# Kernel tuning notes

Hardware: AMD Instinct MI355X
Metric: run time of the kernel (lower is better)

Reference implementation:

```python
import jax, jax.numpy as jnp
import numpy as np

K = 4          # torus_dim (circles)
M = 6          # n_modes
GRID = 12      # grid_size for Laplacian eigenvalues
T = 2.0        # uniformity temperature
SPREAD_W = 1.0
B = 8192       # batch size


def _karmonic_weights():
    # lambda_n = 2 - 2 cos(2 pi n / N), n = 1..M; w = (lam - lam1)/(lam_max - lam1)
    n = np.arange(1, M + 1)
    lam = 2.0 - 2.0 * np.cos(2.0 * np.pi * n / GRID)
    w = (lam - lam[0]) / (lam.max() - lam[0])
    return jnp.asarray(w, dtype=jnp.float32)


def setup_inputs() -> dict:
    key = jax.random.key(0)
    k1, k2 = jax.random.split(key)
    angles = jax.random.normal(k1, (B, K), dtype=jnp.float32)
    fourier_embed = jax.random.normal(k2, (B, 2 * K * M), dtype=jnp.float32)
    return {"angles": angles, "fourier_embed": fourier_embed}


def reference(angles, fourier_embed):
    Bn = fourier_embed.shape[0]
    w = _karmonic_weights()
    # group by mode: (B, M, 2K)
    x = fourier_embed.reshape(Bn, M, 2 * K)
    eye = jnp.eye(Bn, dtype=bool)
    log_Bm1 = jnp.log(jnp.float32(Bn - 1))

    total_unif = jnp.float32(0.0)
    mode_unifs = []
    for n in range(M):  # fixed small structural loop over modes
        xn = x[:, n, :]                                   # (B, 2K)
        sq = jnp.sum(xn * xn, axis=1)                     # (B,)
        d2 = sq[:, None] + sq[None, :] - 2.0 * (xn @ xn.T)
        d2 = jnp.maximum(d2, 0.0)                         # cdist(...)**2, clamped >= 0
        neg = jnp.where(eye, -jnp.inf, -T * d2)           # exclude diagonal like masked_select
        unif_n = jnp.mean(jax.nn.logsumexp(neg, axis=1)) - log_Bm1
        mode_unifs.append(unif_n)
        total_unif = total_unif + w[n] * unif_n

    # circular decorrelation (spread) across circle pairs, vectorized over pairs
    mu = jnp.arctan2(jnp.mean(jnp.sin(angles), axis=0),
                     jnp.mean(jnp.cos(angles), axis=0))   # (K,) circular means
    s = jnp.sin(angles - mu[None, :])                     # (B, K)
    cov = (s.T @ s) / jnp.float32(Bn)                     # (K, K) = mean(s_i * s_j)
    var = jnp.diagonal(cov)                               # mean(s_i^2)
    den = jnp.sqrt(var[:, None] * var[None, :] + 1e-8)
    corr2 = (cov / den) ** 2
    iu = np.triu_indices(K, 1)                            # upper-triangle pairs i<j
    spread = jnp.mean(corr2[iu])

    total = total_unif + jnp.float32(SPREAD_W) * spread
    return total_unif, spread, total, jnp.stack(mode_unifs)
```

## Files before the change

### kernel.cpp

```cpp
#include <hip/hip_runtime.h>
#include <math.h>

constexpr int BN = 8192;
constexpr int MN = 6;

constexpr float TL    = 2.8853900817779268f;
constexpr float SCL_Z = 2.4022448795936154f;

typedef __bf16 bf16_t;
typedef bf16_t bf16x8 __attribute__((ext_vector_type(8)));
typedef float f32x4 __attribute__((ext_vector_type(4)));

union PK { bf16_t h[8]; uint4 u; };

__device__ __forceinline__ bf16x8 frag_of(uint4 u) {
    return __builtin_bit_cast(bf16x8, u);
}

__device__ __host__ __forceinline__ int midx(int a, int b) {
    return 8 * a - (a * (a - 1)) / 2 + (b - a);
}


__global__ __launch_bounds__(256) void prep_ang(const float* __restrict__ x,
                                                const float* __restrict__ ang,
                                                uint4* __restrict__ C,
                                                float* __restrict__ angp) {
    const int blk = blockIdx.x;
    const int tid = threadIdx.x;
    if (blk < 192) {
        int idx = blk * 256 + tid;
        int n = idx >> 13;
        int j = idx & (BN - 1);
        const float* p = x + (size_t)j * 48 + n * 8;

        PK zh, zl, a3, b3;
        float sq = 0.f;
#pragma unroll
        for (int k = 0; k < 8; ++k) {
            float v = p[k];
            sq = fmaf(v, v, sq);
            float z = SCL_Z * v;
            bf16_t h = (bf16_t)z;
            zh.h[k] = h;
            zl.h[k] = (bf16_t)(z - (float)h);
        }
        float s = -TL * sq;
        bf16_t sh = (bf16_t)s;
        bf16_t sl = (bf16_t)(s - (float)sh);
        bf16_t one = (bf16_t)1.0f, zero = (bf16_t)0.0f;
        a3.h[0] = one; a3.h[1] = one; a3.h[2] = sh;  a3.h[3] = sl;
        b3.h[0] = sh;  b3.h[1] = sl;  b3.h[2] = one; b3.h[3] = one;
#pragma unroll
        for (int k = 4; k < 8; ++k) { a3.h[k] = zero; b3.h[k] = zero; }

        size_t base = ((size_t)(n * 512 + (j >> 4))) * 64 + (j & 15);
        C[base +  0] = zh.u;
        C[base + 16] = zl.u;
        C[base + 32] = a3.u;
        C[base + 48] = b3.u;
    } else {
        const int i = (blk - 192) * 256 + tid;
        float v[8];
#pragma unroll
        for (int k = 0; k < 4; ++k) __sincosf(ang[i * 4 + k], &v[k], &v[4 + k]);
        float acc[44];
        int c = 0;
#pragma unroll
        for (int a = 0; a < 8; ++a)
#pragma unroll
            for (int bq = a; bq < 8; ++bq) acc[c++] = v[a] * v[bq];
#pragma unroll
        for (int a = 0; a < 8; ++a) acc[36 + a] = v[a];

#pragma unroll
        for (int q = 0; q < 44; ++q) {
            float s = acc[q];
            s += __shfl_xor(s, 1);  s += __shfl_xor(s, 2);
            s += __shfl_xor(s, 4);  s += __shfl_xor(s, 8);
            s += __shfl_xor(s, 16); s += __shfl_xor(s, 32);
            acc[q] = s;
        }
        __shared__ float sm[4][44];
        const int w = tid >> 6, lane = tid & 63;
        if (lane == 0)
#pragma unroll
            for (int q = 0; q < 44; ++q) sm[w][q] = acc[q];
        __syncthreads();
        if (tid < 44)
            angp[(blk - 192) * 44 + tid] =
                sm[0][tid] + sm[1][tid] + sm[2][tid] + sm[3][tid];
    }
}

__global__ __launch_bounds__(512, 6) void pair_sweep(const uint4* __restrict__ C,
                                                     float* __restrict__ colsumP,
                                                     unsigned short* __restrict__ credP) {
    const int tid  = threadIdx.x;
    const int lane = tid & 63;
    const int w    = __builtin_amdgcn_readfirstlane(tid >> 6);
    const int b    = blockIdx.x;
    const int m    = b >> 7;
    const int sp   = (b >> 1) & 63;
    const int h    = b & 1;
    const int rho  = 2 * w + h;

    __shared__ float cred[8192];
    __shared__ float smem[2][8][64];
    for (int q = tid; q < 8192; q += 512) cred[q] = 0.f;
    __syncthreads();

    const int g  = lane >> 4;
    const int pa = (g == 3) ? 2 : (g & 1);
    const int pb = (g == 3) ? 3 : (g >> 1);
    const int cl = lane & 15;
    const f32x4 z4 = {0.f, 0.f, 0.f, 0.f};
    const uint4* mbase = C + (size_t)m * 512 * 64;
    const uint4* bcol  = mbase + pb * 16 + cl;

#pragma unroll 1
    for (int sidx = 0; sidx < 2; ++sidx) {
        const int s = sidx ? (127 - sp) : sp;

        bf16x8 af[4];
#pragma unroll
        for (int t = 0; t < 4; ++t)
            af[t] = frag_of(mbase[(size_t)(4 * s + t) * 64 + pa * 16 + cl]);

        float racc[16];
#pragma unroll
        for (int q = 0; q < 16; ++q) racc[q] = 0.f;

        const int start = 4 * s + 4;
        const int first = start + (int)(((unsigned)(rho - start)) & 15u);
        const int f0 = (first < 512) ? first : 0;

        uint4 b0 = bcol[(size_t)f0 * 64];
        uint4 b1 = bcol[(size_t)(f0 + 16) * 64];
        for (int jt = first; jt < 512; jt += 16) {
            uint4 p0 = bcol[(size_t)(jt + 32) * 64];
            bf16x8 bf = frag_of(b0);
            float rsum = 0.f;
#pragma unroll
            for (int t = 0; t < 4; ++t) {
                f32x4 d = __builtin_amdgcn_mfma_f32_16x16x32_bf16(af[t], bf, z4, 0, 0, 0);
#pragma unroll
                for (int r = 0; r < 4; ++r) {
                    float e = __builtin_amdgcn_exp2f(d[r]);
                    racc[t * 4 + r] += e;
                    rsum += e;
                }
            }
            rsum += __shfl_xor(rsum, 16);
            rsum += __shfl_xor(rsum, 32);
            if (lane < 16) cred[jt * 16 + lane] += rsum;
            b0 = b1; b1 = p0;
        }

        if (w == 7 - sidx) {
            const int dd = cl - 4 * g;
#pragma unroll
            for (int u = 0; u < 4; ++u) {
                bf16x8 bf = frag_of(mbase[(size_t)(4 * s + u) * 64 + pb * 16 + cl]);
#pragma unroll
                for (int t = 0; t < 4; ++t) {
                    f32x4 d = __builtin_amdgcn_mfma_f32_16x16x32_bf16(af[t], bf, z4, 0, 0, 0);
#pragma unroll
                    for (int r = 0; r < 4; ++r) {
                        float e = __builtin_amdgcn_exp2f(d[r]);
                        if (u == t && dd == r) e = 0.f;
                        racc[t * 4 + r] += e;
                    }
                }
            }
        }

#pragma unroll
        for (int q = 0; q < 16; ++q) {
            float v = racc[q];
            v += __shfl_xor(v, 1);
            v += __shfl_xor(v, 2);
            v += __shfl_xor(v, 4);
            v += __shfl_xor(v, 8);
            racc[q] = v;
        }
        if (cl == 0) {
#pragma unroll
            for (int t = 0; t < 4; ++t)
#pragma unroll
                for (int r = 0; r < 4; ++r)
                    smem[sidx][w][t * 16 + g * 4 + r] = racc[t * 4 + r];
        }
    }

    __syncthreads();

    if (tid < 128) {
        const int si = tid >> 6, row = tid & 63;
        float ssum = 0.f;
#pragma unroll
        for (int ww = 0; ww < 8; ++ww) ssum += smem[si][ww][row];
        const int s = si ? (127 - sp) : sp;
        colsumP[(size_t)h * (MN * BN) + m * BN + s * 64 + row] = ssum;
    }

    for (int q = tid; q < 4096; q += 512) {
        const int jt = 2 * (q >> 4) + h, c = q & 15;
        bf16_t v = (bf16_t)cred[jt * 16 + c];
        credP[(size_t)sp * (MN * BN) + m * BN + jt * 16 + c] =
            __builtin_bit_cast(unsigned short, v);
    }
}

__global__ __launch_bounds__(512) void log_red(const float* __restrict__ colsumP,
                                               const unsigned short* __restrict__ credP,
                                               float* __restrict__ lp) {
    const int tid = threadIdx.x;
    const int idx = blockIdx.x * 512 + tid;

    float v = colsumP[idx] + colsumP[MN * BN + idx];
#pragma unroll 8
    for (int sp = 0; sp < 64; ++sp) {
        unsigned short u = credP[(size_t)sp * (MN * BN) + idx];
        v += (float)__builtin_bit_cast(bf16_t, u);
    }
    float lg = logf(v);
    lg += __shfl_xor(lg, 1);
    lg += __shfl_xor(lg, 2);
    lg += __shfl_xor(lg, 4);
    lg += __shfl_xor(lg, 8);
    lg += __shfl_xor(lg, 16);
    lg += __shfl_xor(lg, 32);
    __shared__ float sm[8];
    if ((tid & 63) == 0) sm[tid >> 6] = lg;
    __syncthreads();
    if (tid == 0) {
        float s = 0.f;
#pragma unroll
        for (int k = 0; k < 8; ++k) s += sm[k];
        lp[blockIdx.x] = s;
    }
}

__global__ __launch_bounds__(64) void final_asm(const float* __restrict__ angp,
                                                const float* __restrict__ lp,
                                                float* __restrict__ out) {
    const int tid = threadIdx.x;
    __shared__ float mom[44];

    if (tid < 44) {
        float s = 0.f;
        for (int bk = 0; bk < 32; ++bk) s += angp[bk * 44 + tid];
        mom[tid] = s;
    }
    __syncthreads();

    if (tid == 0) {
        float sm[4], cm[4];
#pragma unroll
        for (int k = 0; k < 4; ++k) {
            float S = mom[36 + k], Cc = mom[40 + k];
            float hyp = sqrtf(S * S + Cc * Cc);
            sm[k] = S / hyp;
            cm[k] = Cc / hyp;
        }
        auto COV = [&](int k, int l) -> float {
            int ks = k < l ? k : l, kl = k < l ? l : k;
            float mss = mom[midx(ks, kl)];
            float msc_kl = mom[midx(k, l + 4)];
            float msc_lk = mom[midx(l, k + 4)];
            float mcc = mom[midx(ks + 4, kl + 4)];
            return (cm[k] * cm[l] * mss - cm[k] * sm[l] * msc_kl -
                    sm[k] * cm[l] * msc_lk + sm[k] * sm[l] * mcc) *
                   (1.0f / (float)BN);
        };
        float var[4] = {COV(0, 0), COV(1, 1), COV(2, 2), COV(3, 3)};
        float spread = 0.f;
        const int pk[6] = {0, 0, 0, 1, 1, 2};
        const int pl[6] = {1, 2, 3, 2, 3, 3};
#pragma unroll
        for (int p = 0; p < 6; ++p) {
            float cv = COV(pk[p], pl[p]);
            float den = sqrtf(var[pk[p]] * var[pl[p]] + 1e-8f);
            float cr = cv / den;
            spread += cr * cr;
        }
        spread *= (1.0f / 6.0f);

        const float wgt[6] = {0.0f, 0.19615242270663188f, 0.4641016151377544f,
                              0.7320508075688773f, 0.9282032302755088f, 1.0f};
        const float logBm1 = logf((float)(BN - 1));
        float total_unif = 0.f, unif[6];
#pragma unroll
        for (int mm = 0; mm < 6; ++mm) {
            float s = 0.f;
            for (int k = 0; k < 16; ++k) s += lp[mm * 16 + k];
            unif[mm] = s * (1.0f / (float)BN) - logBm1;
            total_unif += wgt[mm] * unif[mm];
        }
        out[0] = total_unif;
        out[1] = spread;
        out[2] = total_unif + spread;
#pragma unroll
        for (int mm = 0; mm < 6; ++mm) out[3 + mm] = unif[mm];
    }
}

extern "C" void kernel_launch(void* const* d_in, const int* in_sizes, int n_in,
                              void* d_out, int out_size, void* d_ws, size_t ws_size,
                              hipStream_t stream) {
    const float* angles  = (const float*)d_in[0];
    const float* fourier = (const float*)d_in[1];
    float* out = (float*)d_out;

    char* ws = (char*)d_ws;
    uint4* C              = (uint4*)(ws + 0);
    unsigned short* credP = (unsigned short*)(ws + 3145728);
    float* colsumP        = (float*)(ws + 9437184);
    float* lp             = (float*)(ws + 9830400);
    float* angp           = (float*)(ws + 9830784);

    prep_ang<<<dim3(224), dim3(256), 0, stream>>>(fourier, angles, C, angp);
    pair_sweep<<<dim3(768), dim3(512), 0, stream>>>(C, colsumP, credP);
    log_red<<<dim3(96), dim3(512), 0, stream>>>(colsumP, credP, lp);
    final_asm<<<dim3(1), dim3(64), 0, stream>>>(angp, lp, out);
}
```

Measured before the change: 62.31 us.

## Move diagonal-block work into reduction kernel and fuse final assembly via last-block atomic

New measurement: 84.32 us. 1.35x slower.

```diff
diff --git a/kernel.cpp b/kernel.cpp
--- a/kernel.cpp
+++ b/kernel.cpp
@@ -157,24 +157,6 @@
             b0 = b1; b1 = p0;
         }
 
-        if (w == 7 - sidx) {
-            const int dd = cl - 4 * g;
-#pragma unroll
-            for (int u = 0; u < 4; ++u) {
-                bf16x8 bf = frag_of(mbase[(size_t)(4 * s + u) * 64 + pb * 16 + cl]);
-#pragma unroll
-                for (int t = 0; t < 4; ++t) {
-                    f32x4 d = __builtin_amdgcn_mfma_f32_16x16x32_bf16(af[t], bf, z4, 0, 0, 0);
-#pragma unroll
-                    for (int r = 0; r < 4; ++r) {
-                        float e = __builtin_amdgcn_exp2f(d[r]);
-                        if (u == t && dd == r) e = 0.f;
-                        racc[t * 4 + r] += e;
-                    }
-                }
-            }
-        }
-
 #pragma unroll
         for (int q = 0; q < 16; ++q) {
             float v = racc[q];
@@ -207,21 +189,92 @@
     for (int q = tid; q < 4096; q += 512) {
         const int jt = 2 * (q >> 4) + h, c = q & 15;
         bf16_t v = (bf16_t)cred[jt * 16 + c];
-        credP[(size_t)sp * (MN * BN) + m * BN + jt * 16 + c] =
+        credP[((size_t)((m * 64 + sp) * 2 + h)) * 4096 + q] =
             __builtin_bit_cast(unsigned short, v);
     }
 }
 
-__global__ __launch_bounds__(512) void log_red(const float* __restrict__ colsumP,
-                                               const unsigned short* __restrict__ credP,
-                                               float* __restrict__ lp) {
-    const int tid = threadIdx.x;
-    const int idx = blockIdx.x * 512 + tid;
-
-    float v = colsumP[idx] + colsumP[MN * BN + idx];
+__global__ __launch_bounds__(512) void log_wedge_final(
+        const uint4* __restrict__ C,
+        const float* __restrict__ colsumP,
+        const unsigned short* __restrict__ credP,
+        const float* __restrict__ angp,
+        float* __restrict__ lp,
+        int* __restrict__ cnt,
+        float* __restrict__ out) {
+    const int tid  = threadIdx.x;
+    const int b    = blockIdx.x;
+    const int m    = b >> 4;
+    const int lane = tid & 63;
+    const int w    = tid >> 6;
+
+    __shared__ float smW[8][64];
+    __shared__ float smR[8];
+    __shared__ int   isLast;
+
+    {
+        const int s  = (b & 15) * 8 + w;
+        const int g  = lane >> 4;
+        const int pa = (g == 3) ? 2 : (g & 1);
+        const int pb = (g == 3) ? 3 : (g >> 1);
+        const int cl = lane & 15;
+        const int dd = cl - 4 * g;
+        const f32x4 z4 = {0.f, 0.f, 0.f, 0.f};
+        const uint4* mbase = C + (size_t)m * 512 * 64;
+
+        bf16x8 af[4];
+#pragma unroll
+        for (int t = 0; t < 4; ++t)
+            af[t] = frag_of(mbase[(size_t)(4 * s + t) * 64 + pa * 16 + cl]);
+
+        float racc[16];
+#pragma unroll
+        for (int q = 0; q < 16; ++q) racc[q] = 0.f;
+
+#pragma unroll
+        for (int u = 0; u < 4; ++u) {
+            bf16x8 bf = frag_of(mbase[(size_t)(4 * s + u) * 64 + pb * 16 + cl]);
+#pragma unroll
+            for (int t = 0; t < 4; ++t) {
+                f32x4 d = __builtin_amdgcn_mfma_f32_16x16x32_bf16(af[t], bf, z4, 0, 0, 0);
+#pragma unroll
+                for (int r = 0; r < 4; ++r) {
+                    float e = __builtin_amdgcn_exp2f(d[r]);
+                    if (u == t && dd == r) e = 0.f;
+                    racc[t * 4 + r] += e;
+                }
+            }
+        }
+#pragma unroll
+        for (int q = 0; q < 16; ++q) {
+            float v = racc[q];
+            v += __shfl_xor(v, 1);
+            v += __shfl_xor(v, 2);
+            v += __shfl_xor(v, 4);
+            v += __shfl_xor(v, 8);
+            racc[q] = v;
+        }
+        if (cl == 0) {
+#pragma unroll
+            for (int t = 0; t < 4; ++t)
+#pragma unroll
+                for (int r = 0; r < 4; ++r)
+                    smW[w][t * 16 + g * 4 + r] = racc[t * 4 + r];
+        }
+    }
+    __syncthreads();
+
+    const int idx = b * 512 + tid;
+    const int i   = idx & (BN - 1);
+    const int jt  = i >> 4, c = i & 15;
+    const int hh  = jt & 1;
+    const int q   = (jt >> 1) * 16 + c;
+
+    float v = colsumP[idx] + colsumP[MN * BN + idx] + smW[w][lane];
+    const unsigned short* basep = credP + ((size_t)(m * 128 + hh)) * 4096 + q;
 #pragma unroll 8
     for (int sp = 0; sp < 64; ++sp) {
-        unsigned short u = credP[(size_t)sp * (MN * BN) + idx];
+        unsigned short u = basep[(size_t)sp * 8192];
         v += (float)__builtin_bit_cast(bf16_t, u);
     }
     float lg = logf(v);
@@ -231,31 +284,31 @@
     lg += __shfl_xor(lg, 8);
     lg += __shfl_xor(lg, 16);
     lg += __shfl_xor(lg, 32);
-    __shared__ float sm[8];
-    if ((tid & 63) == 0) sm[tid >> 6] = lg;
-    __syncthreads();
+    if (lane == 0) smR[w] = lg;
+    __syncthreads();
+
     if (tid == 0) {
         float s = 0.f;
 #pragma unroll
-        for (int k = 0; k < 8; ++k) s += sm[k];
-        lp[blockIdx.x] = s;
-    }
-}
-
-__global__ __launch_bounds__(64) void final_asm(const float* __restrict__ angp,
-                                                const float* __restrict__ lp,
-                                                float* __restrict__ out) {
-    const int tid = threadIdx.x;
-    __shared__ float mom[44];
-
-    if (tid < 44) {
-        float s = 0.f;
-        for (int bk = 0; bk < 32; ++bk) s += angp[bk * 44 + tid];
-        mom[tid] = s;
-    }
-    __syncthreads();
-
-    if (tid == 0) {
+        for (int k = 0; k < 8; ++k) s += smR[k];
+        lp[b] = s;
+        __threadfence();
+        int prev = atomicAdd(cnt, 1);
+        isLast = (prev == 95) ? 1 : 0;
+    }
+    __syncthreads();
+
+    if (isLast && tid == 0) {
+        __threadfence();
+        const volatile float* vlp = lp;
+
+        float mom[44];
+#pragma unroll
+        for (int k = 0; k < 44; ++k) mom[k] = 0.f;
+        for (int bk = 0; bk < 32; ++bk)
+#pragma unroll
+            for (int k = 0; k < 44; ++k) mom[k] += angp[bk * 44 + k];
+
         float sm[4], cm[4];
 #pragma unroll
         for (int k = 0; k < 4; ++k) {
@@ -294,7 +347,7 @@
 #pragma unroll
         for (int mm = 0; mm < 6; ++mm) {
             float s = 0.f;
-            for (int k = 0; k < 16; ++k) s += lp[mm * 16 + k];
+            for (int k = 0; k < 16; ++k) s += vlp[mm * 16 + k];
             unif[mm] = s * (1.0f / (float)BN) - logBm1;
             total_unif += wgt[mm] * unif[mm];
         }
@@ -319,9 +372,11 @@
     float* colsumP        = (float*)(ws + 9437184);
     float* lp             = (float*)(ws + 9830400);
     float* angp           = (float*)(ws + 9830784);
-
+    int*   cnt            = (int*)(ws + 9836416);
+
+    hipMemsetAsync(cnt, 0, sizeof(int), stream);
     prep_ang<<<dim3(224), dim3(256), 0, stream>>>(fourier, angles, C, angp);
     pair_sweep<<<dim3(768), dim3(512), 0, stream>>>(C, colsumP, credP);
-    log_red<<<dim3(96), dim3(512), 0, stream>>>(colsumP, credP, lp);
-    final_asm<<<dim3(1), dim3(64), 0, stream>>>(angp, lp, out);
-}
+    log_wedge_final<<<dim3(96), dim3(512), 0, stream>>>(C, colsumP, credP,
+                                                        angp, lp, cnt, out);
+}
```
